# Kernel optimization log

Hardware: AMD Instinct MI355X
Metric: run time of the kernel (lower is better)

## Reference

```python
import jax, jax.numpy as jnp
import numpy as np

N_NODES = 100000
N_EDGES = 1000000
DIM = 64
BN_EPS = 1e-5


def setup_inputs() -> dict:
    key = jax.random.key(0)
    k_x, k_src, k_off, k_w, k_b = jax.random.split(key, 5)
    x = jax.random.normal(k_x, (N_NODES, DIM), dtype=jnp.float32)
    # Build edges with src != dst so add_remaining_self_loops semantics reduce to
    # appending one self-loop per node (no pre-existing self loops).
    src = jax.random.randint(k_src, (N_EDGES,), 0, N_NODES, dtype=jnp.int64)
    off = jax.random.randint(k_off, (N_EDGES,), 1, N_NODES, dtype=jnp.int64)
    dst = (src + off) % N_NODES
    edge_index = jnp.stack([src, dst], axis=0)
    lin_w = jax.random.normal(k_w, (DIM, DIM), dtype=jnp.float32) * (1.0 / np.sqrt(DIM))
    lin_b = jax.random.normal(k_b, (DIM,), dtype=jnp.float32) * 0.01
    bn_gamma = jnp.ones((DIM,), dtype=jnp.float32)
    bn_beta = jnp.zeros((DIM,), dtype=jnp.float32)
    return {"x": x, "edge_index": edge_index, "lin_w": lin_w, "lin_b": lin_b,
            "bn_gamma": bn_gamma, "bn_beta": bn_beta}


def reference(x, edge_index, lin_w, lin_b, bn_gamma, bn_beta):
    N = x.shape[0]
    loops = jnp.arange(N, dtype=edge_index.dtype)
    src = jnp.concatenate([edge_index[0], loops])  # add_remaining_self_loops
    dst = jnp.concatenate([edge_index[1], loops])
    # edge_weight is rebound to None inside MySAGEConv.forward, so message == x_j
    msgs = jnp.take(x, src, axis=0)                      # [E+N, D] gather
    summed = jax.ops.segment_sum(msgs, dst, num_segments=N)
    deg = jax.ops.segment_sum(jnp.ones_like(dst, dtype=x.dtype), dst, num_segments=N)
    aggr = summed / deg[:, None]                         # scatter-mean (deg >= 1)
    out = aggr @ lin_w.T + lin_b                         # linear
    # BatchNorm1d, training mode (batch stats, biased variance)
    mean = out.mean(axis=0)
    var = out.var(axis=0)
    out = (out - mean) * jax.lax.rsqrt(var + BN_EPS) * bn_gamma + bn_beta
    out = out + x                                        # residual (in_dim == out_dim)
    return jax.nn.relu(out)
```

## Files before the change

kernel.cpp:

```cpp
#include <hip/hip_runtime.h>

#define N_NODES 100000
#define N_EDGES 1000000
#define DIM 64
#define BN_EPS 1e-5f

#define CAP 40
#define SEG_SHIFT 10
#define SEG_NODES 1024
#define NSEG 98
#define SEGCAP 11264
#define BCAP 96
#define EPB 4096
#define NBIN1 245
#define CONV_BLOCKS 3125
#define OVF_CAP 4096
#define WIN 128
#define GATHER_BLOCKS 784

typedef __attribute__((ext_vector_type(8))) short short8_t;
typedef __attribute__((ext_vector_type(4))) float f32x4;

__device__ inline unsigned bf16rne(float f) {
    unsigned u = __float_as_uint(f);
    return (u + 0x7FFFu + ((u >> 16) & 1u)) >> 16;
}
__device__ inline unsigned pack2(float a, float b) {
    return bf16rne(a) | (bf16rne(b) << 16);
}
__device__ inline void unp_add(unsigned d, float& e0, float& e1) {
    e0 += __uint_as_float(d << 16);
    e1 += __uint_as_float(d & 0xFFFF0000u);
}
__device__ inline void add8(float* acc, uint4 v) {
    unp_add(v.x, acc[0], acc[1]);
    unp_add(v.y, acc[2], acc[3]);
    unp_add(v.z, acc[4], acc[5]);
    unp_add(v.w, acc[6], acc[7]);
}

__global__ __launch_bounds__(256) void k_bin1(const int* __restrict__ ei,
                                              const float4* __restrict__ x4,
                                              const float* __restrict__ W,
                                              unsigned* __restrict__ seg_buf,
                                              int* __restrict__ seg_cnt,
                                              int* __restrict__ ovf_cnt,
                                              uint2* __restrict__ ovf,
                                              uint4* __restrict__ xh,
                                              unsigned short* __restrict__ Wb) {
    __shared__ int cnt[NSEG];
    __shared__ int base[NSEG];
    __shared__ unsigned pairs[NSEG][BCAP];

    int b = blockIdx.x;
    if (b == NBIN1 + CONV_BLOCKS) {
        for (int t = threadIdx.x; t < DIM * DIM / 2; t += 256) {
            float2 w2 = ((const float2*)W)[t];
            ((unsigned*)Wb)[t] = pack2(w2.x, w2.y);
        }
        return;
    }
    if (b >= NBIN1) {
        int g = (b - NBIN1) * 256 + threadIdx.x;
        float4 lo = x4[2 * g];
        float4 hi = x4[2 * g + 1];
        uint4 r;
        r.x = pack2(lo.x, lo.y);
        r.y = pack2(lo.z, lo.w);
        r.z = pack2(hi.x, hi.y);
        r.w = pack2(hi.z, hi.w);
        xh[8 + g] = r;
        return;
    }

    for (int t = threadIdx.x; t < NSEG; t += 256) cnt[t] = 0;
    __syncthreads();

    const int base4 = b * (EPB / 4);
#pragma unroll
    for (int k = 0; k < 4; ++k) {
        int i4 = base4 + k * 256 + threadIdx.x;
        if (i4 < N_EDGES / 4) {
            int4 s4 = ((const int4*)ei)[i4];
            int4 d4 = ((const int4*)(ei + N_EDGES))[i4];
            int ss[4] = {s4.x, s4.y, s4.z, s4.w};
            int dd[4] = {d4.x, d4.y, d4.z, d4.w};
#pragma unroll
            for (int q = 0; q < 4; ++q) {
                int seg = (unsigned)dd[q] >> SEG_SHIFT;
                unsigned pk = ((unsigned)(dd[q] & (SEG_NODES - 1)) << 17)
                            | (unsigned)ss[q];
                int p = atomicAdd(&cnt[seg], 1);
                if (p < BCAP) {
                    pairs[seg][p] = pk;
                } else {
                    int g = atomicAdd(ovf_cnt, 1);
                    if (g < OVF_CAP) ovf[g] = make_uint2((unsigned)ss[q], (unsigned)dd[q]);
                }
            }
        }
    }
    __syncthreads();

    if (threadIdx.x < NSEG) {
        int c = min(cnt[threadIdx.x], BCAP);
        base[threadIdx.x] = atomicAdd(&seg_cnt[threadIdx.x], c);
    }
    __syncthreads();

    const int wave = threadIdx.x >> 6, lane = threadIdx.x & 63;
    for (int seg = wave; seg < NSEG; seg += 4) {
        int c = min(cnt[seg], BCAP);
        int bs = base[seg];
        for (int i = lane; i < c; i += 64) {
            int pos = bs + i;
            if (pos < SEGCAP) seg_buf[seg * SEGCAP + pos] = pairs[seg][i];
        }
    }
}

__global__ __launch_bounds__(256) void k_gather_linear(
        const uint4* __restrict__ xh,
        const unsigned* __restrict__ seg_buf,
        const int* __restrict__ seg_cnt,
        const int* __restrict__ ovf_cnt,
        const uint2* __restrict__ ovf,
        const unsigned short* __restrict__ Wb,
        const float* __restrict__ bias,
        float* __restrict__ lin_out,
        float* __restrict__ stats8) {
    __shared__ int lcnt[WIN];
    __shared__ __align__(16) unsigned lists[WIN][CAP];
    __shared__ __align__(16) unsigned short ab[WIN * 72];
    __shared__ float red0[4][32];
    __shared__ float red1[4][32];

    const int lane = threadIdx.x & 63;
    const int wave = threadIdx.x >> 6;
    const int seg = blockIdx.x >> 3;
    const int winbase = (blockIdx.x & 7) * WIN;

    for (int t = threadIdx.x; t < WIN; t += 256) lcnt[t] = 0;
    __syncthreads();

    int n = seg_cnt[seg];
    if (n > SEGCAP) n = SEGCAP;
    const unsigned* sb = seg_buf + seg * SEGCAP;

    auto proc = [&](unsigned p) {
        int wloc = (int)(p >> 17) - winbase;
        if ((unsigned)wloc < (unsigned)WIN) {
            int pos = atomicAdd(&lcnt[wloc], 1);
            if (pos < CAP) lists[wloc][pos] = p & 0x1FFFFu;
        }
    };

    for (int i = threadIdx.x * 4; i < n; i += 1024) {
        uint4 p4;
        if (i + 4 <= n) {
            p4 = *(const uint4*)(sb + i);
        } else {
            p4.x = sb[i];
            p4.y = (i + 1 < n) ? sb[i + 1] : 0xFFFFFFFFu;
            p4.z = (i + 2 < n) ? sb[i + 2] : 0xFFFFFFFFu;
            p4.w = 0xFFFFFFFFu;
        }
        proc(p4.x); proc(p4.y); proc(p4.z); proc(p4.w);
    }
    int oc = *ovf_cnt;
    if (oc > OVF_CAP) oc = OVF_CAP;
    for (int t = threadIdx.x; t < oc; t += 256) {
        uint2 pr = ovf[t];
        if ((int)(pr.y >> SEG_SHIFT) == seg) {
            int wloc = (int)(pr.y & (SEG_NODES - 1)) - winbase;
            if ((unsigned)wloc < (unsigned)WIN) {
                int pos = atomicAdd(&lcnt[wloc], 1);
                if (pos < CAP) lists[wloc][pos] = pr.x;
            }
        }
    }
    __syncthreads();

    const int sub = lane >> 3, f8 = lane & 7;
#pragma unroll
    for (int s = 0; s < 4; ++s) {
        const int r = s * 32 + wave * 8 + sub;
        const int row = blockIdx.x * WIN + r;
        float acc[8] = {0.f, 0.f, 0.f, 0.f, 0.f, 0.f, 0.f, 0.f};
        if (row < N_NODES) add8(acc, xh[(row + 1) * 8 + f8]);

        const int ctrue = lcnt[r];
        const int c = (ctrue < CAP) ? ctrue : CAP;
        const int* sp = (const int*)&lists[r][0];
        for (int i = 0; i < c; i += 4) {
            int4 e = *(const int4*)(sp + i);
            int e1 = (i + 1 < c) ? e.y : -1;
            int e2 = (i + 2 < c) ? e.z : -1;
            int e3 = (i + 3 < c) ? e.w : -1;
            uint4 v0 = xh[(e.x + 1) * 8 + f8];
            uint4 v1 = xh[(e1 + 1) * 8 + f8];
            uint4 v2 = xh[(e2 + 1) * 8 + f8];
            uint4 v3 = xh[(e3 + 1) * 8 + f8];
            add8(acc, v0);
            add8(acc, v1);
            add8(acc, v2);
            add8(acc, v3);
        }

        const float inv = 1.0f / (float)(ctrue + 1);
#pragma unroll
        for (int k = 0; k < 8; ++k) acc[k] *= inv;

        uint4 pk;
        pk.x = pack2(acc[0], acc[1]);
        pk.y = pack2(acc[2], acc[3]);
        pk.z = pack2(acc[4], acc[5]);
        pk.w = pack2(acc[6], acc[7]);
        *(uint4*)&ab[r * 72 + f8 * 8] = pk;
    }
    __syncthreads();

    const int mh = wave & 1, nh = wave >> 1;
    const int m = lane & 15, quad = lane >> 4;

    const unsigned short* bp0 = Wb + (nh * 32 + m) * 64 + quad * 8;
    short8_t b00 = *(const short8_t*)bp0;
    short8_t b01 = *(const short8_t*)(bp0 + 32);
    const unsigned short* bp1 = bp0 + 16 * 64;
    short8_t b10 = *(const short8_t*)bp1;
    short8_t b11 = *(const short8_t*)(bp1 + 32);
    const float bj0 = bias[nh * 32 + m];
    const float bj1 = bias[nh * 32 + 16 + m];

    float t0acc = 0.f, t1acc = 0.f;

#pragma unroll
    for (int s = 0; s < 4; ++s) {
        const unsigned short* ap = &ab[(s * 32 + mh * 16 + m) * 72 + quad * 8];
        short8_t a0 = *(const short8_t*)ap;
        short8_t a1 = *(const short8_t*)(ap + 32);

        f32x4 c0 = {0.f, 0.f, 0.f, 0.f}, c1 = {0.f, 0.f, 0.f, 0.f};
        c0 = __builtin_amdgcn_mfma_f32_16x16x32_bf16(a0, b00, c0, 0, 0, 0);
        c0 = __builtin_amdgcn_mfma_f32_16x16x32_bf16(a1, b01, c0, 0, 0, 0);
        c1 = __builtin_amdgcn_mfma_f32_16x16x32_bf16(a0, b10, c1, 0, 0, 0);
        c1 = __builtin_amdgcn_mfma_f32_16x16x32_bf16(a1, b11, c1, 0, 0, 0);

        const int rb = blockIdx.x * WIN + s * 32 + mh * 16 + quad * 4;
#pragma unroll
        for (int f = 0; f < 2; ++f) {
            f32x4 cc = f ? c1 : c0;
            int col = nh * 32 + f * 16 + m;
            float bj = f ? bj1 : bj0;
            float q0 = 0.f, q1 = 0.f;
#pragma unroll
            for (int rr = 0; rr < 4; ++rr) {
                float v = cc[rr] + bj;
                if (rb + rr < N_NODES) {
                    lin_out[(rb + rr) * DIM + col] = v;
                    q0 += v;
                    q1 += v * v;
                }
            }
            q0 += __shfl_xor(q0, 16); q0 += __shfl_xor(q0, 32);
            q1 += __shfl_xor(q1, 16); q1 += __shfl_xor(q1, 32);
            if (quad == 0) {
                red0[wave][f * 16 + m] = q0;
                red1[wave][f * 16 + m] = q1;
            }
        }
        __syncthreads();
        if (threadIdx.x < DIM) {
            int j = threadIdx.x, jh = j >> 5, jl = j & 31;
            t0acc += red0[2 * jh][jl] + red0[2 * jh + 1][jl];
            t1acc += red1[2 * jh][jl] + red1[2 * jh + 1][jl];
        }
        __syncthreads();
    }

    if (threadIdx.x < DIM) {
        float* sbk = stats8 + (blockIdx.x & 7) * 128;
        atomicAdd(&sbk[threadIdx.x], t0acc);
        atomicAdd(&sbk[DIM + threadIdx.x], t1acc);
    }
}

__global__ __launch_bounds__(256) void k_final(const float4* lin4,
                                               const unsigned short* __restrict__ xh16,
                                               const float* __restrict__ stats8,
                                               const float* __restrict__ gamma,
                                               const float* __restrict__ beta,
                                               float4* out4) {
    __shared__ float ss[2][DIM];
    if (threadIdx.x < DIM) {
        int j = threadIdx.x;
        float s0 = 0.f, s1 = 0.f;
#pragma unroll
        for (int b = 0; b < 8; ++b) {
            s0 += stats8[b * 128 + j];
            s1 += stats8[b * 128 + DIM + j];
        }
        const float invN = 1.0f / (float)N_NODES;
        float mean = s0 * invN;
        float var = s1 * invN - mean * mean;
        float scale = gamma[j] * rsqrtf(var + BN_EPS);
        ss[0][j] = scale;
        ss[1][j] = beta[j] - mean * scale;
    }
    __syncthreads();
    int tid = blockIdx.x * blockDim.x + threadIdx.x;
    int row = tid >> 4;
    int j4 = (tid & 15) * 4;
    float4 l = lin4[tid];
    ushort2 h01 = *(const ushort2*)&xh16[(row + 1) * 64 + j4];
    ushort2 h23 = *(const ushort2*)&xh16[(row + 1) * 64 + j4 + 2];
    float4 o;
    o.x = fmaxf(fmaf(l.x, ss[0][j4 + 0], ss[1][j4 + 0])
                + __uint_as_float((unsigned)h01.x << 16), 0.f);
    o.y = fmaxf(fmaf(l.y, ss[0][j4 + 1], ss[1][j4 + 1])
                + __uint_as_float((unsigned)h01.y << 16), 0.f);
    o.z = fmaxf(fmaf(l.z, ss[0][j4 + 2], ss[1][j4 + 2])
                + __uint_as_float((unsigned)h23.x << 16), 0.f);
    o.w = fmaxf(fmaf(l.w, ss[0][j4 + 3], ss[1][j4 + 3])
                + __uint_as_float((unsigned)h23.y << 16), 0.f);
    out4[tid] = o;
}

extern "C" void kernel_launch(void* const* d_in, const int* in_sizes, int n_in,
                              void* d_out, int out_size, void* d_ws, size_t ws_size,
                              hipStream_t stream) {
    const float* x     = (const float*)d_in[0];
    const int*   ei    = (const int*)d_in[1];
    const float* W     = (const float*)d_in[2];
    const float* bias  = (const float*)d_in[3];
    const float* gamma = (const float*)d_in[4];
    const float* beta  = (const float*)d_in[5];
    float* out = (float*)d_out;

    char* ws = (char*)d_ws;
    float*          stats8  = (float*)(ws);
    int*            seg_cnt = (int*)(ws + 4096);
    int*            ovf_cnt = (int*)(ws + 4608);
    uint2*          ovf     = (uint2*)(ws + 4736);
    uint4*          xh      = (uint4*)(ws + 37504);
    unsigned short* Wb      = (unsigned short*)(ws + 12837632);
    unsigned*       seg_buf = (unsigned*)(ws + 12845824);

    hipMemsetAsync(ws, 0, 37632, stream);

    k_bin1<<<NBIN1 + CONV_BLOCKS + 1, 256, 0, stream>>>(
        ei, (const float4*)x, W, seg_buf, seg_cnt, ovf_cnt, ovf, xh, Wb);

    k_gather_linear<<<GATHER_BLOCKS, 256, 0, stream>>>(
        xh, seg_buf, seg_cnt, ovf_cnt, ovf, Wb, bias, out, stats8);

    k_final<<<N_NODES * (DIM / 4) / 256, 256, 0, stream>>>(
        (const float4*)out, (const unsigned short*)xh, stats8, gamma, beta,
        (float4*)out);
}
```

Before: 143.1 us.

## Fuse binning, gather-linear and batchnorm into one cooperative kernel

Replaces the three-kernel pipeline with a single cooperative kernel of 784 blocks that uses grid-wide syncs between binning, gather+MFMA linear, and the BN/residual/ReLU finalize. The linear output tile is kept in shared memory instead of written to and re-read from global memory, which removes two kernel launches and a full round trip of the intermediate. The cost is that binning now runs with a grid-stride loop over fewer blocks, two grid barriers are added, and occupancy is constrained by the cooperative launch. The old three-kernel path is kept as a fallback if the cooperative launch fails.

```diff
diff --git a/kernel.cpp b/kernel.cpp
--- a/kernel.cpp
+++ b/kernel.cpp
@@ -1,4 +1,7 @@
 #include <hip/hip_runtime.h>
+#include <hip/hip_cooperative_groups.h>
+
+namespace cg = cooperative_groups;
 
 #define N_NODES 100000
 #define N_EDGES 1000000
@@ -11,12 +14,13 @@
 #define NSEG 98
 #define SEGCAP 11264
 #define BCAP 96
+#define OVF_CAP 4096
+#define WIN 128
+#define FUSED_GRID 784
+
 #define EPB 4096
 #define NBIN1 245
 #define CONV_BLOCKS 3125
-#define OVF_CAP 4096
-#define WIN 128
-#define GATHER_BLOCKS 784
 
 typedef __attribute__((ext_vector_type(8))) short short8_t;
 typedef __attribute__((ext_vector_type(4))) float f32x4;
@@ -39,29 +43,49 @@
     unp_add(v.w, acc[6], acc[7]);
 }
 
-__global__ __launch_bounds__(256) void k_bin1(const int* __restrict__ ei,
-                                              const float4* __restrict__ x4,
-                                              const float* __restrict__ W,
-                                              unsigned* __restrict__ seg_buf,
-                                              int* __restrict__ seg_cnt,
-                                              int* __restrict__ ovf_cnt,
-                                              uint2* __restrict__ ovf,
-                                              uint4* __restrict__ xh,
-                                              unsigned short* __restrict__ Wb) {
-    __shared__ int cnt[NSEG];
-    __shared__ int base[NSEG];
-    __shared__ unsigned pairs[NSEG][BCAP];
-
-    int b = blockIdx.x;
-    if (b == NBIN1 + CONV_BLOCKS) {
-        for (int t = threadIdx.x; t < DIM * DIM / 2; t += 256) {
+__global__ __launch_bounds__(256, 4) void k_fused(
+        const int* __restrict__ ei,
+        const float4* __restrict__ x4,
+        const float* __restrict__ W,
+        unsigned* __restrict__ seg_buf,
+        int* __restrict__ seg_cnt,
+        int* __restrict__ ovf_cnt,
+        uint2* __restrict__ ovf,
+        uint4* __restrict__ xh,
+        unsigned short* __restrict__ Wb,
+        const float* __restrict__ bias,
+        const float* __restrict__ gamma,
+        const float* __restrict__ beta,
+        float* __restrict__ stats8,
+        float4* __restrict__ out4) {
+    __shared__ alignas(16) char smem[40448];
+
+    int*            lcnt  = (int*)smem;
+    unsigned (*lists)[CAP] = (unsigned(*)[CAP])(smem + 512);
+    unsigned short* ab    = (unsigned short*)(smem + 20992);
+    float (*red0)[32]     = (float(*)[32])(smem + 39424);
+    float (*red1)[32]     = (float(*)[32])(smem + 39936);
+    int*            cnt   = (int*)smem;
+    int*            bse   = (int*)(smem + 512);
+    unsigned (*pairs)[BCAP] = (unsigned(*)[BCAP])(smem + 1024);
+    float*          lin01 = (float*)(smem + 512);
+    float*          lin23 = (float*)(smem + 20992);
+    float*          pscale = (float*)(smem + 39424);
+    float*          pshift = (float*)(smem + 39680);
+
+    const int tid  = threadIdx.x;
+    const int bid  = blockIdx.x;
+    const int lane = tid & 63;
+    const int wave = tid >> 6;
+    cg::grid_group gg = cg::this_grid();
+
+    if (bid == FUSED_GRID - 1) {
+        for (int t = tid; t < DIM * DIM / 2; t += 256) {
             float2 w2 = ((const float2*)W)[t];
             ((unsigned*)Wb)[t] = pack2(w2.x, w2.y);
         }
-        return;
-    }
-    if (b >= NBIN1) {
-        int g = (b - NBIN1) * 256 + threadIdx.x;
+    }
+    for (int g = bid * 256 + tid; g < N_NODES * DIM / 8; g += FUSED_GRID * 256) {
         float4 lo = x4[2 * g];
         float4 hi = x4[2 * g + 1];
         uint4 r;
@@ -70,77 +94,53 @@
         r.z = pack2(hi.x, hi.y);
         r.w = pack2(hi.z, hi.w);
         xh[8 + g] = r;
-        return;
-    }
-
-    for (int t = threadIdx.x; t < NSEG; t += 256) cnt[t] = 0;
-    __syncthreads();
-
-    const int base4 = b * (EPB / 4);
-#pragma unroll
-    for (int k = 0; k < 4; ++k) {
-        int i4 = base4 + k * 256 + threadIdx.x;
-        if (i4 < N_EDGES / 4) {
-            int4 s4 = ((const int4*)ei)[i4];
-            int4 d4 = ((const int4*)(ei + N_EDGES))[i4];
-            int ss[4] = {s4.x, s4.y, s4.z, s4.w};
-            int dd[4] = {d4.x, d4.y, d4.z, d4.w};
-#pragma unroll
-            for (int q = 0; q < 4; ++q) {
-                int seg = (unsigned)dd[q] >> SEG_SHIFT;
-                unsigned pk = ((unsigned)(dd[q] & (SEG_NODES - 1)) << 17)
-                            | (unsigned)ss[q];
-                int p = atomicAdd(&cnt[seg], 1);
-                if (p < BCAP) {
-                    pairs[seg][p] = pk;
-                } else {
-                    int g = atomicAdd(ovf_cnt, 1);
-                    if (g < OVF_CAP) ovf[g] = make_uint2((unsigned)ss[q], (unsigned)dd[q]);
-                }
-            }
-        }
-    }
-    __syncthreads();
-
-    if (threadIdx.x < NSEG) {
-        int c = min(cnt[threadIdx.x], BCAP);
-        base[threadIdx.x] = atomicAdd(&seg_cnt[threadIdx.x], c);
-    }
-    __syncthreads();
-
-    const int wave = threadIdx.x >> 6, lane = threadIdx.x & 63;
+    }
+
+    for (int t = tid; t < NSEG; t += 256) cnt[t] = 0;
+    __syncthreads();
+
+    for (int i4 = bid * 256 + tid; i4 < N_EDGES / 4; i4 += FUSED_GRID * 256) {
+        int4 s4 = ((const int4*)ei)[i4];
+        int4 d4 = ((const int4*)(ei + N_EDGES))[i4];
+        int ss_[4] = {s4.x, s4.y, s4.z, s4.w};
+        int dd_[4] = {d4.x, d4.y, d4.z, d4.w};
+#pragma unroll
+        for (int q = 0; q < 4; ++q) {
+            int seg = (unsigned)dd_[q] >> SEG_SHIFT;
+            unsigned pk = ((unsigned)(dd_[q] & (SEG_NODES - 1)) << 17)
+                        | (unsigned)ss_[q];
+            int p = atomicAdd(&cnt[seg], 1);
+            if (p < BCAP) {
+                pairs[seg][p] = pk;
+            } else {
+                int g = atomicAdd(ovf_cnt, 1);
+                if (g < OVF_CAP) ovf[g] = make_uint2((unsigned)ss_[q], (unsigned)dd_[q]);
+            }
+        }
+    }
+    __syncthreads();
+
+    if (tid < NSEG) {
+        int c = min(cnt[tid], BCAP);
+        bse[tid] = atomicAdd(&seg_cnt[tid], c);
+    }
+    __syncthreads();
+
     for (int seg = wave; seg < NSEG; seg += 4) {
         int c = min(cnt[seg], BCAP);
-        int bs = base[seg];
+        int b0 = bse[seg];
         for (int i = lane; i < c; i += 64) {
-            int pos = bs + i;
+            int pos = b0 + i;
             if (pos < SEGCAP) seg_buf[seg * SEGCAP + pos] = pairs[seg][i];
         }
     }
-}
-
-__global__ __launch_bounds__(256) void k_gather_linear(
-        const uint4* __restrict__ xh,
-        const unsigned* __restrict__ seg_buf,
-        const int* __restrict__ seg_cnt,
-        const int* __restrict__ ovf_cnt,
-        const uint2* __restrict__ ovf,
-        const unsigned short* __restrict__ Wb,
-        const float* __restrict__ bias,
-        float* __restrict__ lin_out,
-        float* __restrict__ stats8) {
-    __shared__ int lcnt[WIN];
-    __shared__ __align__(16) unsigned lists[WIN][CAP];
-    __shared__ __align__(16) unsigned short ab[WIN * 72];
-    __shared__ float red0[4][32];
-    __shared__ float red1[4][32];
-
-    const int lane = threadIdx.x & 63;
-    const int wave = threadIdx.x >> 6;
-    const int seg = blockIdx.x >> 3;
-    const int winbase = (blockIdx.x & 7) * WIN;
-
-    for (int t = threadIdx.x; t < WIN; t += 256) lcnt[t] = 0;
+
+    gg.sync();
+
+    const int seg = bid >> 3;
+    const int winbase = (bid & 7) * WIN;
+
+    for (int t = tid; t < WIN; t += 256) lcnt[t] = 0;
     __syncthreads();
 
     int n = seg_cnt[seg];
@@ -155,7 +155,7 @@
         }
     };
 
-    for (int i = threadIdx.x * 4; i < n; i += 1024) {
+    for (int i = tid * 4; i < n; i += 1024) {
         uint4 p4;
         if (i + 4 <= n) {
             p4 = *(const uint4*)(sb + i);
@@ -169,7 +169,7 @@
     }
     int oc = *ovf_cnt;
     if (oc > OVF_CAP) oc = OVF_CAP;
-    for (int t = threadIdx.x; t < oc; t += 256) {
+    for (int t = tid; t < oc; t += 256) {
         uint2 pr = ovf[t];
         if ((int)(pr.y >> SEG_SHIFT) == seg) {
             int wloc = (int)(pr.y & (SEG_NODES - 1)) - winbase;
@@ -185,7 +185,7 @@
 #pragma unroll
     for (int s = 0; s < 4; ++s) {
         const int r = s * 32 + wave * 8 + sub;
-        const int row = blockIdx.x * WIN + r;
+        const int row = bid * WIN + r;
         float acc[8] = {0.f, 0.f, 0.f, 0.f, 0.f, 0.f, 0.f, 0.f};
         if (row < N_NODES) add8(acc, xh[(row + 1) * 8 + f8]);
 
@@ -246,6 +246,307 @@
         c1 = __builtin_amdgcn_mfma_f32_16x16x32_bf16(a0, b10, c1, 0, 0, 0);
         c1 = __builtin_amdgcn_mfma_f32_16x16x32_bf16(a1, b11, c1, 0, 0, 0);
 
+        float lv[8];
+        const int rb = bid * WIN + s * 32 + mh * 16 + quad * 4;
+#pragma unroll
+        for (int f = 0; f < 2; ++f) {
+            f32x4 cc = f ? c1 : c0;
+            float bj = f ? bj1 : bj0;
+            float q0 = 0.f, q1 = 0.f;
+#pragma unroll
+            for (int rr = 0; rr < 4; ++rr) {
+                float v = cc[rr] + bj;
+                lv[f * 4 + rr] = v;
+                if (rb + rr < N_NODES) { q0 += v; q1 += v * v; }
+            }
+            q0 += __shfl_xor(q0, 16); q0 += __shfl_xor(q0, 32);
+            q1 += __shfl_xor(q1, 16); q1 += __shfl_xor(q1, 32);
+            if (quad == 0) {
+                red0[wave][f * 16 + m] = q0;
+                red1[wave][f * 16 + m] = q1;
+            }
+        }
+        __syncthreads();
+        if (tid < DIM) {
+            int j = tid, jh = j >> 5, jl = j & 31;
+            t0acc += red0[2 * jh][jl] + red0[2 * jh + 1][jl];
+            t1acc += red1[2 * jh][jl] + red1[2 * jh + 1][jl];
+        }
+        {
+            float* ldst = (s < 2) ? (lin01 + s * 2048) : (lin23 + (s - 2) * 2048);
+            const int rloc = mh * 16 + quad * 4;
+#pragma unroll
+            for (int f = 0; f < 2; ++f) {
+                int col = nh * 32 + f * 16 + m;
+#pragma unroll
+                for (int rr = 0; rr < 4; ++rr)
+                    ldst[(rloc + rr) * 64 + col] = lv[f * 4 + rr];
+            }
+        }
+        __syncthreads();
+    }
+
+    if (tid < DIM) {
+        float* sbk = stats8 + (bid & 7) * 128;
+        atomicAdd(&sbk[tid], t0acc);
+        atomicAdd(&sbk[DIM + tid], t1acc);
+    }
+
+    gg.sync();
+
+    if (tid < DIM) {
+        int j = tid;
+        float s0 = 0.f, s1 = 0.f;
+#pragma unroll
+        for (int b = 0; b < 8; ++b) {
+            s0 += stats8[b * 128 + j];
+            s1 += stats8[b * 128 + DIM + j];
+        }
+        const float invN = 1.0f / (float)N_NODES;
+        float mean = s0 * invN;
+        float var = s1 * invN - mean * mean;
+        float scale = gamma[j] * rsqrtf(var + BN_EPS);
+        pscale[j] = scale;
+        pshift[j] = beta[j] - mean * scale;
+    }
+    __syncthreads();
+
+    const unsigned short* xh16 = (const unsigned short*)xh;
+#pragma unroll
+    for (int it = 0; it < 8; ++it) {
+        int idx = it * 256 + tid;
+        int rloc = idx >> 4;
+        int c4 = (idx & 15) * 4;
+        int row = bid * WIN + rloc;
+        if (row < N_NODES) {
+            int s = rloc >> 5, rr = rloc & 31;
+            const float* lsrc = ((s < 2) ? (lin01 + s * 2048)
+                                         : (lin23 + (s - 2) * 2048))
+                                + rr * 64 + c4;
+            float4 l = *(const float4*)lsrc;
+            ushort2 h01 = *(const ushort2*)&xh16[(row + 1) * 64 + c4];
+            ushort2 h23 = *(const ushort2*)&xh16[(row + 1) * 64 + c4 + 2];
+            float4 o;
+            o.x = fmaxf(fmaf(l.x, pscale[c4 + 0], pshift[c4 + 0])
+                        + __uint_as_float((unsigned)h01.x << 16), 0.f);
+            o.y = fmaxf(fmaf(l.y, pscale[c4 + 1], pshift[c4 + 1])
+                        + __uint_as_float((unsigned)h01.y << 16), 0.f);
+            o.z = fmaxf(fmaf(l.z, pscale[c4 + 2], pshift[c4 + 2])
+                        + __uint_as_float((unsigned)h23.x << 16), 0.f);
+            o.w = fmaxf(fmaf(l.w, pscale[c4 + 3], pshift[c4 + 3])
+                        + __uint_as_float((unsigned)h23.y << 16), 0.f);
+            out4[row * 16 + (idx & 15)] = o;
+        }
+    }
+}
+
+__global__ __launch_bounds__(256) void k_bin1(const int* __restrict__ ei,
+                                              const float4* __restrict__ x4,
+                                              const float* __restrict__ W,
+                                              unsigned* __restrict__ seg_buf,
+                                              int* __restrict__ seg_cnt,
+                                              int* __restrict__ ovf_cnt,
+                                              uint2* __restrict__ ovf,
+                                              uint4* __restrict__ xh,
+                                              unsigned short* __restrict__ Wb) {
+    __shared__ int cnt[NSEG];
+    __shared__ int base[NSEG];
+    __shared__ unsigned pairs[NSEG][BCAP];
+
+    int b = blockIdx.x;
+    if (b == NBIN1 + CONV_BLOCKS) {
+        for (int t = threadIdx.x; t < DIM * DIM / 2; t += 256) {
+            float2 w2 = ((const float2*)W)[t];
+            ((unsigned*)Wb)[t] = pack2(w2.x, w2.y);
+        }
+        return;
+    }
+    if (b >= NBIN1) {
+        int g = (b - NBIN1) * 256 + threadIdx.x;
+        float4 lo = x4[2 * g];
+        float4 hi = x4[2 * g + 1];
+        uint4 r;
+        r.x = pack2(lo.x, lo.y);
+        r.y = pack2(lo.z, lo.w);
+        r.z = pack2(hi.x, hi.y);
+        r.w = pack2(hi.z, hi.w);
+        xh[8 + g] = r;
+        return;
+    }
+
+    for (int t = threadIdx.x; t < NSEG; t += 256) cnt[t] = 0;
+    __syncthreads();
+
+    const int base4 = b * (EPB / 4);
+#pragma unroll
+    for (int k = 0; k < 4; ++k) {
+        int i4 = base4 + k * 256 + threadIdx.x;
+        if (i4 < N_EDGES / 4) {
+            int4 s4 = ((const int4*)ei)[i4];
+            int4 d4 = ((const int4*)(ei + N_EDGES))[i4];
+            int ss[4] = {s4.x, s4.y, s4.z, s4.w};
+            int dd[4] = {d4.x, d4.y, d4.z, d4.w};
+#pragma unroll
+            for (int q = 0; q < 4; ++q) {
+                int seg = (unsigned)dd[q] >> SEG_SHIFT;
+                unsigned pk = ((unsigned)(dd[q] & (SEG_NODES - 1)) << 17)
+                            | (unsigned)ss[q];
+                int p = atomicAdd(&cnt[seg], 1);
+                if (p < BCAP) {
+                    pairs[seg][p] = pk;
+                } else {
+                    int g = atomicAdd(ovf_cnt, 1);
+                    if (g < OVF_CAP) ovf[g] = make_uint2((unsigned)ss[q], (unsigned)dd[q]);
+                }
+            }
+        }
+    }
+    __syncthreads();
+
+    if (threadIdx.x < NSEG) {
+        int c = min(cnt[threadIdx.x], BCAP);
+        base[threadIdx.x] = atomicAdd(&seg_cnt[threadIdx.x], c);
+    }
+    __syncthreads();
+
+    const int wave = threadIdx.x >> 6, lane = threadIdx.x & 63;
+    for (int seg = wave; seg < NSEG; seg += 4) {
+        int c = min(cnt[seg], BCAP);
+        int bs = base[seg];
+        for (int i = lane; i < c; i += 64) {
+            int pos = bs + i;
+            if (pos < SEGCAP) seg_buf[seg * SEGCAP + pos] = pairs[seg][i];
+        }
+    }
+}
+
+__global__ __launch_bounds__(256) void k_gather_linear(
+        const uint4* __restrict__ xh,
+        const unsigned* __restrict__ seg_buf,
+        const int* __restrict__ seg_cnt,
+        const int* __restrict__ ovf_cnt,
+        const uint2* __restrict__ ovf,
+        const unsigned short* __restrict__ Wb,
+        const float* __restrict__ bias,
+        float* __restrict__ lin_out,
+        float* __restrict__ stats8) {
+    __shared__ int lcnt[WIN];
+    __shared__ __align__(16) unsigned lists[WIN][CAP];
+    __shared__ __align__(16) unsigned short ab[WIN * 72];
+    __shared__ float red0[4][32];
+    __shared__ float red1[4][32];
+
+    const int lane = threadIdx.x & 63;
+    const int wave = threadIdx.x >> 6;
+    const int seg = blockIdx.x >> 3;
+    const int winbase = (blockIdx.x & 7) * WIN;
+
+    for (int t = threadIdx.x; t < WIN; t += 256) lcnt[t] = 0;
+    __syncthreads();
+
+    int n = seg_cnt[seg];
+    if (n > SEGCAP) n = SEGCAP;
+    const unsigned* sb = seg_buf + seg * SEGCAP;
+
+    auto proc = [&](unsigned p) {
+        int wloc = (int)(p >> 17) - winbase;
+        if ((unsigned)wloc < (unsigned)WIN) {
+            int pos = atomicAdd(&lcnt[wloc], 1);
+            if (pos < CAP) lists[wloc][pos] = p & 0x1FFFFu;
+        }
+    };
+
+    for (int i = threadIdx.x * 4; i < n; i += 1024) {
+        uint4 p4;
+        if (i + 4 <= n) {
+            p4 = *(const uint4*)(sb + i);
+        } else {
+            p4.x = sb[i];
+            p4.y = (i + 1 < n) ? sb[i + 1] : 0xFFFFFFFFu;
+            p4.z = (i + 2 < n) ? sb[i + 2] : 0xFFFFFFFFu;
+            p4.w = 0xFFFFFFFFu;
+        }
+        proc(p4.x); proc(p4.y); proc(p4.z); proc(p4.w);
+    }
+    int oc = *ovf_cnt;
+    if (oc > OVF_CAP) oc = OVF_CAP;
+    for (int t = threadIdx.x; t < oc; t += 256) {
+        uint2 pr = ovf[t];
+        if ((int)(pr.y >> SEG_SHIFT) == seg) {
+            int wloc = (int)(pr.y & (SEG_NODES - 1)) - winbase;
+            if ((unsigned)wloc < (unsigned)WIN) {
+                int pos = atomicAdd(&lcnt[wloc], 1);
+                if (pos < CAP) lists[wloc][pos] = pr.x;
+            }
+        }
+    }
+    __syncthreads();
+
+    const int sub = lane >> 3, f8 = lane & 7;
+#pragma unroll
+    for (int s = 0; s < 4; ++s) {
+        const int r = s * 32 + wave * 8 + sub;
+        const int row = blockIdx.x * WIN + r;
+        float acc[8] = {0.f, 0.f, 0.f, 0.f, 0.f, 0.f, 0.f, 0.f};
+        if (row < N_NODES) add8(acc, xh[(row + 1) * 8 + f8]);
+
+        const int ctrue = lcnt[r];
+        const int c = (ctrue < CAP) ? ctrue : CAP;
+        const int* sp = (const int*)&lists[r][0];
+        for (int i = 0; i < c; i += 4) {
+            int4 e = *(const int4*)(sp + i);
+            int e1 = (i + 1 < c) ? e.y : -1;
+            int e2 = (i + 2 < c) ? e.z : -1;
+            int e3 = (i + 3 < c) ? e.w : -1;
+            uint4 v0 = xh[(e.x + 1) * 8 + f8];
+            uint4 v1 = xh[(e1 + 1) * 8 + f8];
+            uint4 v2 = xh[(e2 + 1) * 8 + f8];
+            uint4 v3 = xh[(e3 + 1) * 8 + f8];
+            add8(acc, v0);
+            add8(acc, v1);
+            add8(acc, v2);
+            add8(acc, v3);
+        }
+
+        const float inv = 1.0f / (float)(ctrue + 1);
+#pragma unroll
+        for (int k = 0; k < 8; ++k) acc[k] *= inv;
+
+        uint4 pk;
+        pk.x = pack2(acc[0], acc[1]);
+        pk.y = pack2(acc[2], acc[3]);
+        pk.z = pack2(acc[4], acc[5]);
+        pk.w = pack2(acc[6], acc[7]);
+        *(uint4*)&ab[r * 72 + f8 * 8] = pk;
+    }
+    __syncthreads();
+
+    const int mh = wave & 1, nh = wave >> 1;
+    const int m = lane & 15, quad = lane >> 4;
+
+    const unsigned short* bp0 = Wb + (nh * 32 + m) * 64 + quad * 8;
+    short8_t b00 = *(const short8_t*)bp0;
+    short8_t b01 = *(const short8_t*)(bp0 + 32);
+    const unsigned short* bp1 = bp0 + 16 * 64;
+    short8_t b10 = *(const short8_t*)bp1;
+    short8_t b11 = *(const short8_t*)(bp1 + 32);
+    const float bj0 = bias[nh * 32 + m];
+    const float bj1 = bias[nh * 32 + 16 + m];
+
+    float t0acc = 0.f, t1acc = 0.f;
+
+#pragma unroll
+    for (int s = 0; s < 4; ++s) {
+        const unsigned short* ap = &ab[(s * 32 + mh * 16 + m) * 72 + quad * 8];
+        short8_t a0 = *(const short8_t*)ap;
+        short8_t a1 = *(const short8_t*)(ap + 32);
+
+        f32x4 c0 = {0.f, 0.f, 0.f, 0.f}, c1 = {0.f, 0.f, 0.f, 0.f};
+        c0 = __builtin_amdgcn_mfma_f32_16x16x32_bf16(a0, b00, c0, 0, 0, 0);
+        c0 = __builtin_amdgcn_mfma_f32_16x16x32_bf16(a1, b01, c0, 0, 0, 0);
+        c1 = __builtin_amdgcn_mfma_f32_16x16x32_bf16(a0, b10, c1, 0, 0, 0);
+        c1 = __builtin_amdgcn_mfma_f32_16x16x32_bf16(a1, b11, c1, 0, 0, 0);
+
         const int rb = blockIdx.x * WIN + s * 32 + mh * 16 + quad * 4;
 #pragma unroll
         for (int f = 0; f < 2; ++f) {
@@ -348,13 +649,36 @@
 
     hipMemsetAsync(ws, 0, 37632, stream);
 
-    k_bin1<<<NBIN1 + CONV_BLOCKS + 1, 256, 0, stream>>>(
-        ei, (const float4*)x, W, seg_buf, seg_cnt, ovf_cnt, ovf, xh, Wb);
-
-    k_gather_linear<<<GATHER_BLOCKS, 256, 0, stream>>>(
-        xh, seg_buf, seg_cnt, ovf_cnt, ovf, Wb, bias, out, stats8);
-
-    k_final<<<N_NODES * (DIM / 4) / 256, 256, 0, stream>>>(
-        (const float4*)out, (const unsigned short*)xh, stats8, gamma, beta,
-        (float4*)out);
-}
+    const int*      a_ei    = ei;
+    const float4*   a_x4    = (const float4*)x;
+    const float*    a_W     = W;
+    unsigned*       a_segb  = seg_buf;
+    int*            a_segc  = seg_cnt;
+    int*            a_ovfc  = ovf_cnt;
+    uint2*          a_ovf   = ovf;
+    uint4*          a_xh    = xh;
+    unsigned short* a_Wb    = Wb;
+    const float*    a_bias  = bias;
+    const float*    a_gamma = gamma;
+    const float*    a_beta  = beta;
+    float*          a_st    = stats8;
+    float4*         a_out   = (float4*)out;
+    void* args[] = {(void*)&a_ei, (void*)&a_x4, (void*)&a_W, (void*)&a_segb,
+                    (void*)&a_segc, (void*)&a_ovfc, (void*)&a_ovf, (void*)&a_xh,
+                    (void*)&a_Wb, (void*)&a_bias, (void*)&a_gamma, (void*)&a_beta,
+                    (void*)&a_st, (void*)&a_out};
+    hipError_t err = hipLaunchCooperativeKernel(
+        reinterpret_cast<void*>(k_fused), dim3(FUSED_GRID), dim3(256),
+        args, 0, stream);
+
+    if (err != hipSuccess) {
+        (void)hipGetLastError();
+        k_bin1<<<NBIN1 + CONV_BLOCKS + 1, 256, 0, stream>>>(
+            ei, (const float4*)x, W, seg_buf, seg_cnt, ovf_cnt, ovf, xh, Wb);
+        k_gather_linear<<<NSEG * (SEG_NODES / WIN), 256, 0, stream>>>(
+            xh, seg_buf, seg_cnt, ovf_cnt, ovf, Wb, bias, out, stats8);
+        k_final<<<N_NODES * (DIM / 4) / 256, 256, 0, stream>>>(
+            (const float4*)out, (const unsigned short*)xh, stats8, gamma, beta,
+            (float4*)out);
+    }
+}
```

Measured after the change: 302.4 us. 111% more time.
